# Kernel optimization log

Measured on AMD Instinct MI355X. Metric: run time of the kernel, lower is better.

Reference implementation:

```python
import jax, jax.numpy as jnp
import numpy as np

B, R, C, W, HEADS = 4, 32, 96, 4, 4
SHIFT = W // 2
N = W ** 3                      # tokens per window = 64
NW = (R // W) ** 3              # windows per sample = 512
MLP = 4 * C
EPS = 1e-5


def _build_attn_mask():
    img = np.zeros((R, R, R), dtype=np.float32)
    slices = (slice(0, -W), slice(-W, -SHIFT), slice(-SHIFT, None))
    cnt = 0
    for xs in slices:
        for ys in slices:
            for zs in slices:
                img[xs, ys, zs] = cnt
                cnt += 1
    m = img.reshape(R // W, W, R // W, W, R // W, W)
    m = m.transpose(0, 2, 4, 1, 3, 5).reshape(NW, N)          # (nW, N)
    diff = m[:, None, :] - m[:, :, None]                       # (nW, N, N)
    return np.where(diff != 0, -100.0, 0.0).astype(np.float32)


def setup_inputs() -> dict:
    key = jax.random.key(0)
    ks = jax.random.split(key, 8)
    s = 0.02
    return {
        "inputs": jax.random.normal(ks[0], (B, R ** 3, C), jnp.float32),
        "norm1_g": jnp.ones((C,), jnp.float32),
        "norm1_b": jnp.zeros((C,), jnp.float32),
        "qkv_w": jax.random.normal(ks[1], (C, 3 * C), jnp.float32) * s,
        "qkv_b": jnp.zeros((3 * C,), jnp.float32),
        "proj_w": jax.random.normal(ks[2], (C, C), jnp.float32) * s,
        "proj_b": jnp.zeros((C,), jnp.float32),
        "norm2_g": jnp.ones((C,), jnp.float32),
        "norm2_b": jnp.zeros((C,), jnp.float32),
        "mlp_w1": jax.random.normal(ks[3], (C, MLP), jnp.float32) * s,
        "mlp_b1": jnp.zeros((MLP,), jnp.float32),
        "mlp_w2": jax.random.normal(ks[4], (MLP, C), jnp.float32) * s,
        "mlp_b2": jnp.zeros((C,), jnp.float32),
        "attn_mask": jnp.asarray(_build_attn_mask()),
    }


def _layernorm(x, g, b):
    mu = jnp.mean(x, axis=-1, keepdims=True)
    var = jnp.mean(jnp.square(x - mu), axis=-1, keepdims=True)
    return (x - mu) * jax.lax.rsqrt(var + EPS) * g + b


def _box_partition(x):
    # (B, R, R, R, C) -> (B*nW, N, C)
    x = x.reshape(B, R // W, W, R // W, W, R // W, W, C)
    x = x.transpose(0, 1, 3, 5, 2, 4, 6, 7)
    return x.reshape(-1, N, C)


def _box_reverse(boxes):
    # (B*nW, N, C) -> (B, R, R, R, C)
    x = boxes.reshape(B, R // W, R // W, R // W, W, W, W, C)
    x = x.transpose(0, 1, 4, 2, 5, 3, 6, 7)
    return x.reshape(B, R, R, R, C)


def _forward(inputs, norm1_g, norm1_b, qkv_w, qkv_b, proj_w, proj_b,
             norm2_g, norm2_b, mlp_w1, mlp_b1, mlp_w2, mlp_b2, attn_mask):
    shortcut = inputs
    x = _layernorm(inputs, norm1_g, norm1_b)
    x = x.reshape(B, R, R, R, C)
    x = jnp.roll(x, shift=(-SHIFT, -SHIFT, -SHIFT), axis=(1, 2, 3))
    boxes = _box_partition(x)                                   # (B*nW, N, C)

    dh = C // HEADS
    qkv = boxes @ qkv_w + qkv_b                                 # (B*nW, N, 3C)
    qkv = qkv.reshape(-1, N, 3, HEADS, dh)
    q, k, v = qkv[:, :, 0], qkv[:, :, 1], qkv[:, :, 2]          # (B*nW, N, H, dh)
    scale = dh ** -0.5
    attn = jnp.einsum('wnhd,wmhd->whnm', q, k) * scale          # (B*nW, H, N, N)
    attn = attn.reshape(B, NW, HEADS, N, N) + attn_mask[None, :, None]
    attn = jax.nn.softmax(attn.reshape(-1, HEADS, N, N), axis=-1)
    out = jnp.einsum('whnm,wmhd->wnhd', attn, v).reshape(-1, N, C)
    out = out @ proj_w + proj_b                                 # (B*nW, N, C)

    x = _box_reverse(out)
    x = jnp.roll(x, shift=(SHIFT, SHIFT, SHIFT), axis=(1, 2, 3))
    x = x.reshape(B, R ** 3, C)
    x = x * 0.5 + shortcut                                      # drop_path=0 -> identity

    h = _layernorm(x, norm2_g, norm2_b)
    h = jax.nn.gelu(h @ mlp_w1 + mlp_b1) @ mlp_w2 + mlp_b2
    return h * 0.5 + x


def reference(inputs, norm1_g, norm1_b, qkv_w, qkv_b, proj_w, proj_b,
              norm2_g, norm2_b, mlp_w1, mlp_b1, mlp_w2, mlp_b2, attn_mask):
    return _forward(inputs, norm1_g, norm1_b, qkv_w, qkv_b, proj_w, proj_b,
                    norm2_g, norm2_b, mlp_w1, mlp_b1, mlp_w2, mlp_b2, attn_mask)
```

## Files before the change

### kernel.cpp

```cpp
#include <hip/hip_runtime.h>
#include <hip/hip_bf16.h>

#define CC 96
#define LDXP 104
#define KOFF 6656
#define XOFF 6656
#define VST 72

typedef __bf16 bf16;
typedef __attribute__((ext_vector_type(8))) __bf16 bf16x8;
typedef __attribute__((ext_vector_type(4))) float f32x4;

#define MFMA16(a, b, c) __builtin_amdgcn_mfma_f32_16x16x32_bf16(a, b, c, 0, 0, 0)

__device__ __attribute__((aligned(16))) bf16 g_w1t[384 * 96];
__device__ __attribute__((aligned(16))) bf16 g_w2t[96 * 384];
__device__ __attribute__((aligned(16))) bf16 g_qkvwt[288 * 96];
__device__ __attribute__((aligned(16))) bf16 g_projwt[96 * 96];

template<bool BF>
__device__ __forceinline__ float ldg(const void* p, size_t i) {
    if constexpr (BF) return (float)((const bf16*)p)[i];
    else              return ((const float*)p)[i];
}

template<bool BF>
__device__ __forceinline__ void ld24(const void* p, size_t base, float* v) {
    if constexpr (BF) {
        const bf16* q = (const bf16*)p + base;
        #pragma unroll
        for (int i = 0; i < 3; i++) {
            bf16x8 f = *(const bf16x8*)(q + i * 8);
            #pragma unroll
            for (int j = 0; j < 8; j++) v[i * 8 + j] = (float)f[j];
        }
    } else {
        #pragma unroll
        for (int i = 0; i < 24; i++) v[i] = ((const float*)p)[base + i];
    }
}

__device__ __forceinline__ void st24_lds(bf16* dst, const float* v) {
    #pragma unroll
    for (int i = 0; i < 3; i++) {
        bf16x8 f;
        #pragma unroll
        for (int j = 0; j < 8; j++) f[j] = (bf16)v[i * 8 + j];
        *(bf16x8*)(dst + i * 8) = f;
    }
}

template<bool BF>
__device__ __forceinline__ void st24_glob(const bf16* stage, void* out, size_t g) {
    if constexpr (BF) {
        #pragma unroll
        for (int i = 0; i < 3; i++)
            *(bf16x8*)((bf16*)out + g + i * 8) = *(const bf16x8*)(stage + i * 8);
    } else {
        #pragma unroll
        for (int i = 0; i < 6; i++) {
            f32x4 v;
            #pragma unroll
            for (int j = 0; j < 4; j++) v[j] = (float)stage[i * 4 + j];
            *(f32x4*)((float*)out + g + i * 4) = v;
        }
    }
}

__device__ __forceinline__ bf16x8 ldsA(const bf16* base, int row0, int ld, int k0) {
    const int l = threadIdx.x & 63;
    return *(const bf16x8*)(base + (row0 + (l & 15)) * ld + k0 + (l >> 4) * 8);
}
__device__ __forceinline__ bf16x8 gB(const bf16* base, int n0, int K, int k0) {
    const int l = threadIdx.x & 63;
    return *(const bf16x8*)(base + (n0 + (l & 15)) * K + k0 + (l >> 4) * 8);
}

__device__ __forceinline__ float gelu_f(float x) {
    const float s = x * x;
    const float r = x * __builtin_fmaf(0.044715f, s, 1.0f);
    return x * __builtin_amdgcn_rcpf(1.0f + __expf(-1.5957691216057308f * r));
}

template<bool BF>
__device__ void tbody(int idx, const void* qkv_w, const void* proj_w,
                      const void* w1, const void* w2) {
    if (idx < 384 * 96) {
        int n = idx / 96, k = idx % 96;
        g_w1t[idx] = (bf16)ldg<BF>(w1, (size_t)k * 384 + n);
    } else if (idx < 2 * 384 * 96) {
        int j = idx - 384 * 96; int n = j / 384, k = j % 384;
        g_w2t[j] = (bf16)ldg<BF>(w2, (size_t)k * 96 + n);
    } else if (idx < 2 * 384 * 96 + 288 * 96) {
        int j = idx - 2 * 384 * 96; int n = j / 96, k = j % 96;
        g_qkvwt[j] = (bf16)ldg<BF>(qkv_w, (size_t)k * 288 + n);
    } else {
        int j = idx - 2 * 384 * 96 - 288 * 96;
        if (j < 96 * 96) {
            int n = j / 96, k = j % 96;
            g_projwt[j] = (bf16)ldg<BF>(proj_w, (size_t)k * 96 + n);
        }
    }
}
__global__ __launch_bounds__(256) void transpose_kernel(
    const void* g1, const void* qkv_w, const void* proj_w, const void* w1, const void* w2) {
    const int idx = blockIdx.x * 256 + threadIdx.x;
    if (((const unsigned*)g1)[0] == 0x3F803F80u) tbody<true >(idx, qkv_w, proj_w, w1, w2);
    else                                         tbody<false>(idx, qkv_w, proj_w, w1, w2);
}

template<bool BF>
__device__ void fused_body(const void* x_in, const void* g1v, const void* b1v,
                           const void* qkv_b, const void* proj_b,
                           const void* g2v, const void* b2v, const void* mb1,
                           const void* mb2, void* out,
                           bf16* bufA, bf16* bufX, int* src_s)
{
    const int t = threadIdx.x;
    const int w = t >> 6;
    const int l = t & 63;
    const int box = blockIdx.x;
    const int b = box >> 9, bx = (box >> 6) & 7, by = (box >> 3) & 7, bz = box & 7;
    const bool b7x = (bx == 7), b7y = (by == 7), b7z = (bz == 7);
    const bool boundary = b7x || b7y || b7z;
    auto gc = [&](int n) -> int {
        return ((b7x && (n & 32)) ? 4 : 0) | ((b7y && (n & 8)) ? 2 : 0)
             | ((b7z && (n & 2)) ? 1 : 0);
    };
    const int qkvS = w * 4 + (w < 2 ? w : 2), qkvC = 5 - (w >> 1);
    const int sixS = w + (w < 2 ? w : 2),     sixC = 2 - (w >> 1);

    bf16x8 resid[3];

    if (t < 64) *(f32x4*)(bufX + t * LDXP + 96) = (f32x4){0.f, 0.f, 0.f, 0.f};

    {
        const int row = t >> 2, quad = t & 3;
        const int wx = row >> 4, wy = (row >> 2) & 3, wz = row & 3;
        const int sx = (bx * 4 + wx + 2) & 31;
        const int sy = (by * 4 + wy + 2) & 31;
        const int sz = (bz * 4 + wz + 2) & 31;
        const int src = ((b * 32 + sx) * 32 + sy) * 32 + sz;
        if (quad == 0) src_s[row] = src;
        float v[24];
        ld24<BF>(x_in, (size_t)src * CC + quad * 24, v);
        #pragma unroll
        for (int i = 0; i < 3; i++) {
            bf16x8 f;
            #pragma unroll
            for (int j = 0; j < 8; j++) f[j] = (bf16)v[i * 8 + j];
            resid[i] = f;
        }
        float s = 0.f, ss = 0.f;
        #pragma unroll
        for (int i = 0; i < 24; i++) { s += v[i]; ss += v[i] * v[i]; }
        s += __shfl_xor(s, 1);  ss += __shfl_xor(ss, 1);
        s += __shfl_xor(s, 2);  ss += __shfl_xor(ss, 2);
        const float mu = s * (1.f / 96.f);
        const float rstd = rsqrtf(ss * (1.f / 96.f) - mu * mu + 1e-5f);
        float o[24];
        #pragma unroll
        for (int i = 0; i < 24; i++) {
            const int c = quad * 24 + i;
            o[i] = (v[i] - mu) * rstd * ldg<BF>(g1v, c) + ldg<BF>(b1v, c);
        }
        st24_lds(bufA + row * LDXP + quad * 24, o);
    }
    __syncthreads();

    {
        bf16x8 aF[12];
        #pragma unroll
        for (int qt = 0; qt < 4; qt++)
            #pragma unroll
            for (int k = 0; k < 3; k++)
                aF[qt * 3 + k] = ldsA(bufA, qt * 16, LDXP, k * 32);
        __syncthreads();

        for (int i = 0; i < qkvC; i++) {
            const int nt = qkvS + i;
            const bf16x8 bB0 = gB(g_qkvwt, nt * 16, 96, 0);
            const bf16x8 bB1 = gB(g_qkvwt, nt * 16, 96, 32);
            const bf16x8 bB2 = gB(g_qkvwt, nt * 16, 96, 64);
            const int col = nt * 16 + (l & 15);
            const float bias = ldg<BF>(qkv_b, col);
            #pragma unroll
            for (int qt = 0; qt < 4; qt++) {
                f32x4 acc = {0.f, 0.f, 0.f, 0.f};
                acc = MFMA16(aF[qt * 3 + 0], bB0, acc);
                acc = MFMA16(aF[qt * 3 + 1], bB1, acc);
                acc = MFMA16(aF[qt * 3 + 2], bB2, acc);
                const int rq = qt * 16 + ((l >> 4) << 2);
                if (nt < 6) {
                    #pragma unroll
                    for (int r = 0; r < 4; r++)
                        bufX[(rq + r) * LDXP + col] = (bf16)(acc[r] + bias);
                } else if (nt < 12) {
                    const int c = col - 96;
                    #pragma unroll
                    for (int r = 0; r < 4; r++)
                        bufX[KOFF + (rq + r) * LDXP + c] = (bf16)(acc[r] + bias);
                } else {
                    const int c = col - 192;
                    #pragma unroll
                    for (int r = 0; r < 4; r++)
                        bufA[c * VST + rq + r] = (bf16)(acc[r] + bias);
                }
            }
        }
    }
    __syncthreads();

    {
        const int h = w;
        bf16x8 aQ[4], bK[4], bV[2][2];
        #pragma unroll
        for (int qt = 0; qt < 4; qt++)
            aQ[qt] = *(const bf16x8*)(bufX + (qt * 16 + (l & 15)) * LDXP + h * 24 + ((l >> 4) << 3));
        #pragma unroll
        for (int mt = 0; mt < 4; mt++) {
            if (l < 48) {
                bK[mt] = *(const bf16x8*)(bufX + KOFF + (mt * 16 + (l & 15)) * LDXP
                                          + h * 24 + ((l >> 4) << 3));
            } else {
                bf16x8 z;
                #pragma unroll
                for (int j = 0; j < 8; j++) z[j] = (bf16)0.f;
                bK[mt] = z;
            }
        }
        #pragma unroll
        for (int ks = 0; ks < 2; ks++)
            #pragma unroll
            for (int nt = 0; nt < 2; nt++)
                bV[ks][nt] = *(const bf16x8*)(bufA + (h * 24 + nt * 8 + (l & 15)) * VST
                                              + ks * 32 + ((l >> 4) << 3));
        __syncthreads();

        f32x4 S[4][4];
        #pragma unroll
        for (int qt = 0; qt < 4; qt++)
            #pragma unroll
            for (int mt = 0; mt < 4; mt++)
                S[qt][mt] = MFMA16(aQ[qt], bK[mt], ((f32x4){0.f, 0.f, 0.f, 0.f}));

        {
            const int row = t >> 2, quad = t & 3;
            #pragma unroll
            for (int i = 0; i < 3; i++)
                *(bf16x8*)(bufX + XOFF + row * LDXP + quad * 24 + i * 8) = resid[i];
        }

        const float scale = 0.20412414523193154f;
        bf16* pB = bufX + h * 1024;
        int gcol[4];
        if (boundary) {
            #pragma unroll
            for (int mt = 0; mt < 4; mt++) gcol[mt] = gc(mt * 16 + (l & 15));
        }
        #pragma unroll
        for (int qt = 0; qt < 4; qt++) {
            float e[4][4], rs[4] = {0.f, 0.f, 0.f, 0.f};
            if (boundary) {
                int grow[4];
                #pragma unroll
                for (int r = 0; r < 4; r++)
                    grow[r] = gc(qt * 16 + ((l >> 4) << 2) + r);
                #pragma unroll
                for (int mt = 0; mt < 4; mt++)
                    #pragma unroll
                    for (int r = 0; r < 4; r++) {
                        float ev = __expf(S[qt][mt][r] * scale);
                        ev = (grow[r] == gcol[mt]) ? ev : 0.f;
                        e[mt][r] = ev; rs[r] += ev;
                    }
            } else {
                #pragma unroll
                for (int mt = 0; mt < 4; mt++)
                    #pragma unroll
                    for (int r = 0; r < 4; r++) {
                        const float ev = __expf(S[qt][mt][r] * scale);
                        e[mt][r] = ev; rs[r] += ev;
                    }
            }
            #pragma unroll
            for (int r = 0; r < 4; r++) {
                rs[r] += __shfl_xor(rs[r], 1);
                rs[r] += __shfl_xor(rs[r], 2);
                rs[r] += __shfl_xor(rs[r], 4);
                rs[r] += __shfl_xor(rs[r], 8);
            }
            float ri[4];
            #pragma unroll
            for (int r = 0; r < 4; r++) ri[r] = __builtin_amdgcn_rcpf(rs[r]);
            #pragma unroll
            for (int mt = 0; mt < 4; mt++) {
                const int colm = mt * 16 + (l & 15);
                const int chl = colm >> 3;
                #pragma unroll
                for (int r = 0; r < 4; r++) {
                    const int lr = ((l >> 4) << 2) + r;
                    const int ch = chl ^ (lr & 7);
                    pB[lr * 64 + ch * 8 + (colm & 7)] = (bf16)(e[mt][r] * ri[r]);
                }
            }
            f32x4 Oq0 = {0.f, 0.f, 0.f, 0.f}, Oq1 = {0.f, 0.f, 0.f, 0.f};
            #pragma unroll
            for (int ks = 0; ks < 2; ks++) {
                const int lr2 = l & 15;
                const int ch = (ks * 4 + (l >> 4)) ^ (lr2 & 7);
                const bf16x8 aP = *(const bf16x8*)(pB + lr2 * 64 + ch * 8);
                Oq0 = MFMA16(aP, bV[ks][0], Oq0);
                Oq1 = MFMA16(aP, bV[ks][1], Oq1);
            }
            #pragma unroll
            for (int nt = 0; nt < 2; nt++) {
                const int cl = nt * 8 + (l & 15);
                if (nt == 0 || (l & 15) >= 8) {
                    const f32x4 Ov = nt ? Oq1 : Oq0;
                    #pragma unroll
                    for (int r = 0; r < 4; r++) {
                        const int row = qt * 16 + ((l >> 4) << 2) + r;
                        bufA[row * LDXP + h * 24 + cl] = (bf16)Ov[r];
                    }
                }
            }
        }
    }
    __syncthreads();

    {
        bf16x8 pF[12];
        #pragma unroll
        for (int qt = 0; qt < 4; qt++)
            #pragma unroll
            for (int k = 0; k < 3; k++)
                pF[qt * 3 + k] = ldsA(bufA, qt * 16, LDXP, k * 32);

        for (int i = 0; i < sixC; i++) {
            const int nt = sixS + i;
            const bf16x8 bB0 = gB(g_projwt, nt * 16, 96, 0);
            const bf16x8 bB1 = gB(g_projwt, nt * 16, 96, 32);
            const bf16x8 bB2 = gB(g_projwt, nt * 16, 96, 64);
            const int col = nt * 16 + (l & 15);
            const float bias = ldg<BF>(proj_b, col);
            #pragma unroll
            for (int qt = 0; qt < 4; qt++) {
                f32x4 acc = {0.f, 0.f, 0.f, 0.f};
                acc = MFMA16(pF[qt * 3 + 0], bB0, acc);
                acc = MFMA16(pF[qt * 3 + 1], bB1, acc);
                acc = MFMA16(pF[qt * 3 + 2], bB2, acc);
                const int rq = qt * 16 + ((l >> 4) << 2);
                #pragma unroll
                for (int r = 0; r < 4; r++) {
                    const int idx = XOFF + (rq + r) * LDXP + col;
                    const float x2v = 0.5f * (acc[r] + bias) + (float)bufX[idx];
                    bufX[idx] = (bf16)x2v;
                }
            }
        }
    }
    __syncthreads();

    {
        const int row = t >> 2, quad = t & 3;
        float v[24];
        #pragma unroll
        for (int i = 0; i < 3; i++) {
            bf16x8 f = *(const bf16x8*)(bufX + XOFF + row * LDXP + quad * 24 + i * 8);
            #pragma unroll
            for (int j = 0; j < 8; j++) v[i * 8 + j] = (float)f[j];
        }
        float s = 0.f, ss = 0.f;
        #pragma unroll
        for (int i = 0; i < 24; i++) { s += v[i]; ss += v[i] * v[i]; }
        s += __shfl_xor(s, 1);  ss += __shfl_xor(ss, 1);
        s += __shfl_xor(s, 2);  ss += __shfl_xor(ss, 2);
        const float mu = s * (1.f / 96.f);
        const float rstd = rsqrtf(ss * (1.f / 96.f) - mu * mu + 1e-5f);
        float o[24];
        #pragma unroll
        for (int i = 0; i < 24; i++) {
            const int c = quad * 24 + i;
            o[i] = (v[i] - mu) * rstd * ldg<BF>(g2v, c) + ldg<BF>(b2v, c);
        }
        st24_lds(bufX + row * LDXP + quad * 24, o);
    }
    __syncthreads();

    {
        bf16x8 mF[12];
        #pragma unroll
        for (int qt = 0; qt < 4; qt++)
            #pragma unroll
            for (int k = 0; k < 3; k++)
                mF[qt * 3 + k] = ldsA(bufX, qt * 16, LDXP, k * 32);

        f32x4 C[2][4];
        #pragma unroll
        for (int i = 0; i < 2; i++)
            #pragma unroll
            for (int qt = 0; qt < 4; qt++) C[i][qt] = (f32x4){0.f, 0.f, 0.f, 0.f};

        for (int c = 0; c < 4; c++) {
            if (c) __syncthreads();
            for (int i = 0; i < sixC; i++) {
                const int lt = sixS + i;
                const int n0 = c * 96 + lt * 16;
                const bf16x8 bB0 = gB(g_w1t, n0, 96, 0);
                const bf16x8 bB1 = gB(g_w1t, n0, 96, 32);
                const bf16x8 bB2 = gB(g_w1t, n0, 96, 64);
                const int colc = lt * 16 + (l & 15);
                const float bias = ldg<BF>(mb1, c * 96 + colc);
                #pragma unroll
                for (int qt = 0; qt < 4; qt++) {
                    f32x4 acc = {0.f, 0.f, 0.f, 0.f};
                    acc = MFMA16(mF[qt * 3 + 0], bB0, acc);
                    acc = MFMA16(mF[qt * 3 + 1], bB1, acc);
                    acc = MFMA16(mF[qt * 3 + 2], bB2, acc);
                    const int rq = qt * 16 + ((l >> 4) << 2);
                    #pragma unroll
                    for (int r = 0; r < 4; r++)
                        bufA[(rq + r) * LDXP + colc] = (bf16)gelu_f(acc[r] + bias);
                }
            }
            __syncthreads();
            bf16x8 hF[12];
            #pragma unroll
            for (int qt = 0; qt < 4; qt++) {
                hF[qt * 3 + 0] = ldsA(bufA, qt * 16, LDXP, 0);
                hF[qt * 3 + 1] = ldsA(bufA, qt * 16, LDXP, 32);
                hF[qt * 3 + 2] = ldsA(bufA, qt * 16, LDXP, 64);
            }
            for (int i = 0; i < sixC; i++) {
                const int ot = sixS + i;
                const bf16x8 bB0 = gB(g_w2t, ot * 16, 384, c * 96);
                const bf16x8 bB1 = gB(g_w2t, ot * 16, 384, c * 96 + 32);
                const bf16x8 bB2 = gB(g_w2t, ot * 16, 384, c * 96 + 64);
                #pragma unroll
                for (int qt = 0; qt < 4; qt++) {
                    C[i][qt] = MFMA16(hF[qt * 3 + 0], bB0, C[i][qt]);
                    C[i][qt] = MFMA16(hF[qt * 3 + 1], bB1, C[i][qt]);
                    C[i][qt] = MFMA16(hF[qt * 3 + 2], bB2, C[i][qt]);
                }
            }
        }
        __syncthreads();

        for (int i = 0; i < sixC; i++) {
            const int ot = sixS + i;
            const int col = ot * 16 + (l & 15);
            const float bias = ldg<BF>(mb2, col);
            #pragma unroll
            for (int qt = 0; qt < 4; qt++) {
                const int rq = qt * 16 + ((l >> 4) << 2);
                #pragma unroll
                for (int r = 0; r < 4; r++) {
                    const float res = (float)bufX[XOFF + (rq + r) * LDXP + col];
                    bufA[(rq + r) * LDXP + col] = (bf16)(0.5f * (C[i][qt][r] + bias) + res);
                }
            }
        }
        __syncthreads();
        {
            const int row = t >> 2, quad = t & 3;
            st24_glob<BF>(bufA + row * LDXP + quad * 24, out,
                          (size_t)src_s[row] * CC + quad * 24);
        }
    }
}

__global__ __launch_bounds__(256, 3) void fused_kernel(
    const void* x_in, const void* g1, const void* b1, const void* qkv_b,
    const void* proj_b, const void* g2, const void* b2,
    const void* mb1, const void* mb2, void* out) {
    __shared__ bf16 bufA[6912];
    __shared__ bf16 bufX[13312];
    __shared__ int src_s[64];
    if (((const unsigned*)g1)[0] == 0x3F803F80u)
        fused_body<true >(x_in, g1, b1, qkv_b, proj_b, g2, b2, mb1, mb2, out,
                          bufA, bufX, src_s);
    else
        fused_body<false>(x_in, g1, b1, qkv_b, proj_b, g2, b2, mb1, mb2, out,
                          bufA, bufX, src_s);
}

extern "C" void kernel_launch(void* const* d_in, const int* in_sizes, int n_in,
                              void* d_out, int out_size, void* d_ws, size_t ws_size,
                              hipStream_t stream) {
    const void* x_in   = d_in[0];
    const void* g1     = d_in[1];
    const void* b1     = d_in[2];
    const void* qkv_w  = d_in[3];
    const void* qkv_b  = d_in[4];
    const void* proj_w = d_in[5];
    const void* proj_b = d_in[6];
    const void* g2     = d_in[7];
    const void* b2     = d_in[8];
    const void* w1     = d_in[9];
    const void* bias1  = d_in[10];
    const void* w2     = d_in[11];
    const void* bias2  = d_in[12];

    transpose_kernel<<<432, 256, 0, stream>>>(g1, qkv_w, proj_w, w1, w2);
    fused_kernel<<<2048, 256, 0, stream>>>(x_in, g1, b1, qkv_b, proj_b,
                                           g2, b2, bias1, bias2, d_out);
}
```

Baseline: 212.0 us.

## Prefetch weight fragments across barriers and double-buffer loads in GEMM phases

Weight fragments and biases for the QKV, projection and MLP GEMMs are now loaded from global memory before the preceding barrier, or double-buffered one tile ahead. The per-wave tile loops are specialised on compile-time counts so they fully unroll. LayerNorm gamma and beta are loaded as vectors up front instead of one element at a time, and the fp32 input load is vectorised to float4. The aim is to hide global-load latency behind barriers and MFMA work, at the cost of more live registers and a possible drop in occupancy.

```diff
diff --git a/kernel.cpp b/kernel.cpp
--- a/kernel.cpp
+++ b/kernel.cpp
@@ -13,6 +13,8 @@
 
 #define MFMA16(a, b, c) __builtin_amdgcn_mfma_f32_16x16x32_bf16(a, b, c, 0, 0, 0)
 
+template<int N> struct icN { static constexpr int value = N; };
+
 __device__ __attribute__((aligned(16))) bf16 g_w1t[384 * 96];
 __device__ __attribute__((aligned(16))) bf16 g_w2t[96 * 384];
 __device__ __attribute__((aligned(16))) bf16 g_qkvwt[288 * 96];
@@ -35,8 +37,13 @@
             for (int j = 0; j < 8; j++) v[i * 8 + j] = (float)f[j];
         }
     } else {
-        #pragma unroll
-        for (int i = 0; i < 24; i++) v[i] = ((const float*)p)[base + i];
+        const float* q = (const float*)p + base;
+        #pragma unroll
+        for (int i = 0; i < 6; i++) {
+            f32x4 f = *(const f32x4*)(q + i * 4);
+            #pragma unroll
+            for (int j = 0; j < 4; j++) v[i * 4 + j] = f[j];
+        }
     }
 }
 
@@ -142,8 +149,10 @@
         const int sz = (bz * 4 + wz + 2) & 31;
         const int src = ((b * 32 + sx) * 32 + sy) * 32 + sz;
         if (quad == 0) src_s[row] = src;
-        float v[24];
+        float v[24], gv[24], bvv[24];
         ld24<BF>(x_in, (size_t)src * CC + quad * 24, v);
+        ld24<BF>(g1v, quad * 24, gv);
+        ld24<BF>(b1v, quad * 24, bvv);
         #pragma unroll
         for (int i = 0; i < 3; i++) {
             bf16x8 f;
@@ -160,12 +169,14 @@
         const float rstd = rsqrtf(ss * (1.f / 96.f) - mu * mu + 1e-5f);
         float o[24];
         #pragma unroll
-        for (int i = 0; i < 24; i++) {
-            const int c = quad * 24 + i;
-            o[i] = (v[i] - mu) * rstd * ldg<BF>(g1v, c) + ldg<BF>(b1v, c);
-        }
+        for (int i = 0; i < 24; i++)
+            o[i] = (v[i] - mu) * rstd * gv[i] + bvv[i];
         st24_lds(bufA + row * LDXP + quad * 24, o);
     }
+    bf16x8 q0f[3]; float q0b;
+    #pragma unroll
+    for (int k = 0; k < 3; k++) q0f[k] = gB(g_qkvwt, qkvS * 16, 96, k * 32);
+    q0b = ldg<BF>(qkv_b, qkvS * 16 + (l & 15));
     __syncthreads();
 
     {
@@ -177,37 +188,51 @@
                 aF[qt * 3 + k] = ldsA(bufA, qt * 16, LDXP, k * 32);
         __syncthreads();
 
-        for (int i = 0; i < qkvC; i++) {
-            const int nt = qkvS + i;
-            const bf16x8 bB0 = gB(g_qkvwt, nt * 16, 96, 0);
-            const bf16x8 bB1 = gB(g_qkvwt, nt * 16, 96, 32);
-            const bf16x8 bB2 = gB(g_qkvwt, nt * 16, 96, 64);
-            const int col = nt * 16 + (l & 15);
-            const float bias = ldg<BF>(qkv_b, col);
-            #pragma unroll
-            for (int qt = 0; qt < 4; qt++) {
-                f32x4 acc = {0.f, 0.f, 0.f, 0.f};
-                acc = MFMA16(aF[qt * 3 + 0], bB0, acc);
-                acc = MFMA16(aF[qt * 3 + 1], bB1, acc);
-                acc = MFMA16(aF[qt * 3 + 2], bB2, acc);
-                const int rq = qt * 16 + ((l >> 4) << 2);
-                if (nt < 6) {
-                    #pragma unroll
-                    for (int r = 0; r < 4; r++)
-                        bufX[(rq + r) * LDXP + col] = (bf16)(acc[r] + bias);
-                } else if (nt < 12) {
-                    const int c = col - 96;
-                    #pragma unroll
-                    for (int r = 0; r < 4; r++)
-                        bufX[KOFF + (rq + r) * LDXP + c] = (bf16)(acc[r] + bias);
-                } else {
-                    const int c = col - 192;
-                    #pragma unroll
-                    for (int r = 0; r < 4; r++)
-                        bufA[c * VST + rq + r] = (bf16)(acc[r] + bias);
-                }
-            }
-        }
+        auto qkv_phase = [&](auto cc) {
+            constexpr int CNT = decltype(cc)::value;
+            bf16x8 fb[2][3]; float bb[2];
+            #pragma unroll
+            for (int k = 0; k < 3; k++) fb[0][k] = q0f[k];
+            bb[0] = q0b;
+            #pragma unroll
+            for (int i = 0; i < CNT; i++) {
+                constexpr int dummy = 0; (void)dummy;
+                const int cur = i & 1, nxt = cur ^ 1;
+                if (i + 1 < CNT) {
+                    #pragma unroll
+                    for (int k = 0; k < 3; k++)
+                        fb[nxt][k] = gB(g_qkvwt, (qkvS + i + 1) * 16, 96, k * 32);
+                    bb[nxt] = ldg<BF>(qkv_b, (qkvS + i + 1) * 16 + (l & 15));
+                }
+                const int nt = qkvS + i;
+                const int col = nt * 16 + (l & 15);
+                #pragma unroll
+                for (int qt = 0; qt < 4; qt++) {
+                    f32x4 acc = {0.f, 0.f, 0.f, 0.f};
+                    acc = MFMA16(aF[qt * 3 + 0], fb[cur][0], acc);
+                    acc = MFMA16(aF[qt * 3 + 1], fb[cur][1], acc);
+                    acc = MFMA16(aF[qt * 3 + 2], fb[cur][2], acc);
+                    const int rq = qt * 16 + ((l >> 4) << 2);
+                    if (nt < 6) {
+                        #pragma unroll
+                        for (int r = 0; r < 4; r++)
+                            bufX[(rq + r) * LDXP + col] = (bf16)(acc[r] + bb[cur]);
+                    } else if (nt < 12) {
+                        const int c = col - 96;
+                        #pragma unroll
+                        for (int r = 0; r < 4; r++)
+                            bufX[KOFF + (rq + r) * LDXP + c] = (bf16)(acc[r] + bb[cur]);
+                    } else {
+                        const int c = col - 192;
+                        #pragma unroll
+                        for (int r = 0; r < 4; r++)
+                            bufA[c * VST + rq + r] = (bf16)(acc[r] + bb[cur]);
+                    }
+                }
+            }
+        };
+        if (w < 2) qkv_phase(icN<5>{});
+        else       qkv_phase(icN<4>{});
     }
     __syncthreads();
 
@@ -327,6 +352,21 @@
             }
         }
     }
+    bf16x8 pjB[2][3]; float pjb[2];
+    {
+        auto pload = [&](auto cc) {
+            constexpr int CNT = decltype(cc)::value;
+            #pragma unroll
+            for (int i = 0; i < CNT; i++) {
+                #pragma unroll
+                for (int k = 0; k < 3; k++)
+                    pjB[i][k] = gB(g_projwt, (sixS + i) * 16, 96, k * 32);
+                pjb[i] = ldg<BF>(proj_b, (sixS + i) * 16 + (l & 15));
+            }
+        };
+        if (w < 2) pload(icN<2>{});
+        else       pload(icN<1>{});
+    }
     __syncthreads();
 
     {
@@ -337,40 +377,44 @@
             for (int k = 0; k < 3; k++)
                 pF[qt * 3 + k] = ldsA(bufA, qt * 16, LDXP, k * 32);
 
-        for (int i = 0; i < sixC; i++) {
-            const int nt = sixS + i;
-            const bf16x8 bB0 = gB(g_projwt, nt * 16, 96, 0);
-            const bf16x8 bB1 = gB(g_projwt, nt * 16, 96, 32);
-            const bf16x8 bB2 = gB(g_projwt, nt * 16, 96, 64);
-            const int col = nt * 16 + (l & 15);
-            const float bias = ldg<BF>(proj_b, col);
-            #pragma unroll
-            for (int qt = 0; qt < 4; qt++) {
-                f32x4 acc = {0.f, 0.f, 0.f, 0.f};
-                acc = MFMA16(pF[qt * 3 + 0], bB0, acc);
-                acc = MFMA16(pF[qt * 3 + 1], bB1, acc);
-                acc = MFMA16(pF[qt * 3 + 2], bB2, acc);
-                const int rq = qt * 16 + ((l >> 4) << 2);
-                #pragma unroll
-                for (int r = 0; r < 4; r++) {
-                    const int idx = XOFF + (rq + r) * LDXP + col;
-                    const float x2v = 0.5f * (acc[r] + bias) + (float)bufX[idx];
-                    bufX[idx] = (bf16)x2v;
-                }
-            }
-        }
+        auto proj_phase = [&](auto cc) {
+            constexpr int CNT = decltype(cc)::value;
+            #pragma unroll
+            for (int i = 0; i < CNT; i++) {
+                const int nt = sixS + i;
+                const int col = nt * 16 + (l & 15);
+                #pragma unroll
+                for (int qt = 0; qt < 4; qt++) {
+                    f32x4 acc = {0.f, 0.f, 0.f, 0.f};
+                    acc = MFMA16(pF[qt * 3 + 0], pjB[i][0], acc);
+                    acc = MFMA16(pF[qt * 3 + 1], pjB[i][1], acc);
+                    acc = MFMA16(pF[qt * 3 + 2], pjB[i][2], acc);
+                    const int rq = qt * 16 + ((l >> 4) << 2);
+                    #pragma unroll
+                    for (int r = 0; r < 4; r++) {
+                        const int idx = XOFF + (rq + r) * LDXP + col;
+                        const float x2v = 0.5f * (acc[r] + pjb[i]) + (float)bufX[idx];
+                        bufX[idx] = (bf16)x2v;
+                    }
+                }
+            }
+        };
+        if (w < 2) proj_phase(icN<2>{});
+        else       proj_phase(icN<1>{});
     }
     __syncthreads();
 
     {
         const int row = t >> 2, quad = t & 3;
-        float v[24];
+        float v[24], gv[24], bvv[24];
         #pragma unroll
         for (int i = 0; i < 3; i++) {
             bf16x8 f = *(const bf16x8*)(bufX + XOFF + row * LDXP + quad * 24 + i * 8);
             #pragma unroll
             for (int j = 0; j < 8; j++) v[i * 8 + j] = (float)f[j];
         }
+        ld24<BF>(g2v, quad * 24, gv);
+        ld24<BF>(b2v, quad * 24, bvv);
         float s = 0.f, ss = 0.f;
         #pragma unroll
         for (int i = 0; i < 24; i++) { s += v[i]; ss += v[i] * v[i]; }
@@ -380,10 +424,8 @@
         const float rstd = rsqrtf(ss * (1.f / 96.f) - mu * mu + 1e-5f);
         float o[24];
         #pragma unroll
-        for (int i = 0; i < 24; i++) {
-            const int c = quad * 24 + i;
-            o[i] = (v[i] - mu) * rstd * ldg<BF>(g2v, c) + ldg<BF>(b2v, c);
-        }
+        for (int i = 0; i < 24; i++)
+            o[i] = (v[i] - mu) * rstd * gv[i] + bvv[i];
         st24_lds(bufX + row * LDXP + quad * 24, o);
     }
     __syncthreads();
@@ -402,48 +444,70 @@
             #pragma unroll
             for (int qt = 0; qt < 4; qt++) C[i][qt] = (f32x4){0.f, 0.f, 0.f, 0.f};
 
+        #pragma unroll
         for (int c = 0; c < 4; c++) {
+            bf16x8 fb[2][3]; float bb[2];
+            #pragma unroll
+            for (int k = 0; k < 3; k++)
+                fb[0][k] = gB(g_w1t, c * 96 + sixS * 16, 96, k * 32);
+            bb[0] = ldg<BF>(mb1, c * 96 + sixS * 16 + (l & 15));
             if (c) __syncthreads();
-            for (int i = 0; i < sixC; i++) {
-                const int lt = sixS + i;
-                const int n0 = c * 96 + lt * 16;
-                const bf16x8 bB0 = gB(g_w1t, n0, 96, 0);
-                const bf16x8 bB1 = gB(g_w1t, n0, 96, 32);
-                const bf16x8 bB2 = gB(g_w1t, n0, 96, 64);
-                const int colc = lt * 16 + (l & 15);
-                const float bias = ldg<BF>(mb1, c * 96 + colc);
+            auto mlp1_seg = [&](auto cc) {
+                constexpr int CNT = decltype(cc)::value;
+                #pragma unroll
+                for (int i = 0; i < CNT; i++) {
+                    const int cur = i & 1, nxt = cur ^ 1;
+                    if (i + 1 < CNT) {
+                        #pragma unroll
+                        for (int k = 0; k < 3; k++)
+                            fb[nxt][k] = gB(g_w1t, c * 96 + (sixS + i + 1) * 16, 96, k * 32);
+                        bb[nxt] = ldg<BF>(mb1, c * 96 + (sixS + i + 1) * 16 + (l & 15));
+                    }
+                    const int colc = (sixS + i) * 16 + (l & 15);
+                    #pragma unroll
+                    for (int qt = 0; qt < 4; qt++) {
+                        f32x4 acc = {0.f, 0.f, 0.f, 0.f};
+                        acc = MFMA16(mF[qt * 3 + 0], fb[cur][0], acc);
+                        acc = MFMA16(mF[qt * 3 + 1], fb[cur][1], acc);
+                        acc = MFMA16(mF[qt * 3 + 2], fb[cur][2], acc);
+                        const int rq = qt * 16 + ((l >> 4) << 2);
+                        #pragma unroll
+                        for (int r = 0; r < 4; r++)
+                            bufA[(rq + r) * LDXP + colc] = (bf16)gelu_f(acc[r] + bb[cur]);
+                    }
+                }
+            };
+            if (w < 2) mlp1_seg(icN<2>{});
+            else       mlp1_seg(icN<1>{});
+            bf16x8 w2f[2][3];
+            auto w2load = [&](auto cc) {
+                constexpr int CNT = decltype(cc)::value;
+                #pragma unroll
+                for (int i = 0; i < CNT; i++)
+                    #pragma unroll
+                    for (int k = 0; k < 3; k++)
+                        w2f[i][k] = gB(g_w2t, (sixS + i) * 16, 384, c * 96 + k * 32);
+            };
+            if (w < 2) w2load(icN<2>{});
+            else       w2load(icN<1>{});
+            __syncthreads();
+            auto mlp2_seg = [&](auto cc) {
+                constexpr int CNT = decltype(cc)::value;
                 #pragma unroll
                 for (int qt = 0; qt < 4; qt++) {
-                    f32x4 acc = {0.f, 0.f, 0.f, 0.f};
-                    acc = MFMA16(mF[qt * 3 + 0], bB0, acc);
-                    acc = MFMA16(mF[qt * 3 + 1], bB1, acc);
-                    acc = MFMA16(mF[qt * 3 + 2], bB2, acc);
-                    const int rq = qt * 16 + ((l >> 4) << 2);
-                    #pragma unroll
-                    for (int r = 0; r < 4; r++)
-                        bufA[(rq + r) * LDXP + colc] = (bf16)gelu_f(acc[r] + bias);
-                }
-            }
-            __syncthreads();
-            bf16x8 hF[12];
-            #pragma unroll
-            for (int qt = 0; qt < 4; qt++) {
-                hF[qt * 3 + 0] = ldsA(bufA, qt * 16, LDXP, 0);
-                hF[qt * 3 + 1] = ldsA(bufA, qt * 16, LDXP, 32);
-                hF[qt * 3 + 2] = ldsA(bufA, qt * 16, LDXP, 64);
-            }
-            for (int i = 0; i < sixC; i++) {
-                const int ot = sixS + i;
-                const bf16x8 bB0 = gB(g_w2t, ot * 16, 384, c * 96);
-                const bf16x8 bB1 = gB(g_w2t, ot * 16, 384, c * 96 + 32);
-                const bf16x8 bB2 = gB(g_w2t, ot * 16, 384, c * 96 + 64);
-                #pragma unroll
-                for (int qt = 0; qt < 4; qt++) {
-                    C[i][qt] = MFMA16(hF[qt * 3 + 0], bB0, C[i][qt]);
-                    C[i][qt] = MFMA16(hF[qt * 3 + 1], bB1, C[i][qt]);
-                    C[i][qt] = MFMA16(hF[qt * 3 + 2], bB2, C[i][qt]);
-                }
-            }
+                    const bf16x8 h0 = ldsA(bufA, qt * 16, LDXP, 0);
+                    const bf16x8 h1 = ldsA(bufA, qt * 16, LDXP, 32);
+                    const bf16x8 h2 = ldsA(bufA, qt * 16, LDXP, 64);
+                    #pragma unroll
+                    for (int i = 0; i < CNT; i++) {
+                        C[i][qt] = MFMA16(h0, w2f[i][0], C[i][qt]);
+                        C[i][qt] = MFMA16(h1, w2f[i][1], C[i][qt]);
+                        C[i][qt] = MFMA16(h2, w2f[i][2], C[i][qt]);
+                    }
+                }
+            };
+            if (w < 2) mlp2_seg(icN<2>{});
+            else       mlp2_seg(icN<1>{});
         }
         __syncthreads();
 
```

After: 248.5 us. 1.17x slower.

## Prefetch weight fragments across GEMM tiles and vectorize LayerNorm param loads

Applied to the files above, without the earlier changes.

Loads the next tile's global weight fragments and bias one iteration early in the QKV, projection and MLP-up loops, and issues the first tile's loads before the preceding barrier. This hides global-load latency behind the MFMA work. The MLP-down weights are loaded before the barrier, and the hidden fragments are read per row tile instead of being held in a 12-register array, which drops that array. The fp32 input path and the LayerNorm gamma/beta now use vector f32x4 loads into registers instead of scalar per-element loads. The prefetched fragments raise register pressure, which could hurt occupancy at the 3-blocks launch bound.

```diff
diff --git a/kernel.cpp b/kernel.cpp
--- a/kernel.cpp
+++ b/kernel.cpp
@@ -35,8 +35,13 @@
             for (int j = 0; j < 8; j++) v[i * 8 + j] = (float)f[j];
         }
     } else {
-        #pragma unroll
-        for (int i = 0; i < 24; i++) v[i] = ((const float*)p)[base + i];
+        const float* q = (const float*)p + base;
+        #pragma unroll
+        for (int i = 0; i < 6; i++) {
+            f32x4 f = *(const f32x4*)(q + i * 4);
+            #pragma unroll
+            for (int j = 0; j < 4; j++) v[i * 4 + j] = f[j];
+        }
     }
 }
 
@@ -142,8 +147,10 @@
         const int sz = (bz * 4 + wz + 2) & 31;
         const int src = ((b * 32 + sx) * 32 + sy) * 32 + sz;
         if (quad == 0) src_s[row] = src;
-        float v[24];
+        float v[24], gv[24], bvv[24];
         ld24<BF>(x_in, (size_t)src * CC + quad * 24, v);
+        ld24<BF>(g1v, quad * 24, gv);
+        ld24<BF>(b1v, quad * 24, bvv);
         #pragma unroll
         for (int i = 0; i < 3; i++) {
             bf16x8 f;
@@ -160,12 +167,14 @@
         const float rstd = rsqrtf(ss * (1.f / 96.f) - mu * mu + 1e-5f);
         float o[24];
         #pragma unroll
-        for (int i = 0; i < 24; i++) {
-            const int c = quad * 24 + i;
-            o[i] = (v[i] - mu) * rstd * ldg<BF>(g1v, c) + ldg<BF>(b1v, c);
-        }
+        for (int i = 0; i < 24; i++)
+            o[i] = (v[i] - mu) * rstd * gv[i] + bvv[i];
         st24_lds(bufA + row * LDXP + quad * 24, o);
     }
+    bf16x8 cf0 = gB(g_qkvwt, qkvS * 16, 96, 0);
+    bf16x8 cf1 = gB(g_qkvwt, qkvS * 16, 96, 32);
+    bf16x8 cf2 = gB(g_qkvwt, qkvS * 16, 96, 64);
+    float   cb = ldg<BF>(qkv_b, qkvS * 16 + (l & 15));
     __syncthreads();
 
     {
@@ -178,35 +187,39 @@
         __syncthreads();
 
         for (int i = 0; i < qkvC; i++) {
+            bf16x8 nf0 = cf0, nf1 = cf1, nf2 = cf2; float nb = cb;
+            if (i + 1 < qkvC) {
+                nf0 = gB(g_qkvwt, (qkvS + i + 1) * 16, 96, 0);
+                nf1 = gB(g_qkvwt, (qkvS + i + 1) * 16, 96, 32);
+                nf2 = gB(g_qkvwt, (qkvS + i + 1) * 16, 96, 64);
+                nb  = ldg<BF>(qkv_b, (qkvS + i + 1) * 16 + (l & 15));
+            }
             const int nt = qkvS + i;
-            const bf16x8 bB0 = gB(g_qkvwt, nt * 16, 96, 0);
-            const bf16x8 bB1 = gB(g_qkvwt, nt * 16, 96, 32);
-            const bf16x8 bB2 = gB(g_qkvwt, nt * 16, 96, 64);
             const int col = nt * 16 + (l & 15);
-            const float bias = ldg<BF>(qkv_b, col);
             #pragma unroll
             for (int qt = 0; qt < 4; qt++) {
                 f32x4 acc = {0.f, 0.f, 0.f, 0.f};
-                acc = MFMA16(aF[qt * 3 + 0], bB0, acc);
-                acc = MFMA16(aF[qt * 3 + 1], bB1, acc);
-                acc = MFMA16(aF[qt * 3 + 2], bB2, acc);
+                acc = MFMA16(aF[qt * 3 + 0], cf0, acc);
+                acc = MFMA16(aF[qt * 3 + 1], cf1, acc);
+                acc = MFMA16(aF[qt * 3 + 2], cf2, acc);
                 const int rq = qt * 16 + ((l >> 4) << 2);
                 if (nt < 6) {
                     #pragma unroll
                     for (int r = 0; r < 4; r++)
-                        bufX[(rq + r) * LDXP + col] = (bf16)(acc[r] + bias);
+                        bufX[(rq + r) * LDXP + col] = (bf16)(acc[r] + cb);
                 } else if (nt < 12) {
                     const int c = col - 96;
                     #pragma unroll
                     for (int r = 0; r < 4; r++)
-                        bufX[KOFF + (rq + r) * LDXP + c] = (bf16)(acc[r] + bias);
+                        bufX[KOFF + (rq + r) * LDXP + c] = (bf16)(acc[r] + cb);
                 } else {
                     const int c = col - 192;
                     #pragma unroll
                     for (int r = 0; r < 4; r++)
-                        bufA[c * VST + rq + r] = (bf16)(acc[r] + bias);
-                }
-            }
+                        bufA[c * VST + rq + r] = (bf16)(acc[r] + cb);
+                }
+            }
+            cf0 = nf0; cf1 = nf1; cf2 = nf2; cb = nb;
         }
     }
     __syncthreads();
@@ -327,6 +340,10 @@
             }
         }
     }
+    bf16x8 pc0 = gB(g_projwt, sixS * 16, 96, 0);
+    bf16x8 pc1 = gB(g_projwt, sixS * 16, 96, 32);
+    bf16x8 pc2 = gB(g_projwt, sixS * 16, 96, 64);
+    float  pcb = ldg<BF>(proj_b, sixS * 16 + (l & 15));
     __syncthreads();
 
     {
@@ -338,39 +355,45 @@
                 pF[qt * 3 + k] = ldsA(bufA, qt * 16, LDXP, k * 32);
 
         for (int i = 0; i < sixC; i++) {
+            bf16x8 nf0 = pc0, nf1 = pc1, nf2 = pc2; float nb = pcb;
+            if (i + 1 < sixC) {
+                nf0 = gB(g_projwt, (sixS + i + 1) * 16, 96, 0);
+                nf1 = gB(g_projwt, (sixS + i + 1) * 16, 96, 32);
+                nf2 = gB(g_projwt, (sixS + i + 1) * 16, 96, 64);
+                nb  = ldg<BF>(proj_b, (sixS + i + 1) * 16 + (l & 15));
+            }
             const int nt = sixS + i;
-            const bf16x8 bB0 = gB(g_projwt, nt * 16, 96, 0);
-            const bf16x8 bB1 = gB(g_projwt, nt * 16, 96, 32);
-            const bf16x8 bB2 = gB(g_projwt, nt * 16, 96, 64);
             const int col = nt * 16 + (l & 15);
-            const float bias = ldg<BF>(proj_b, col);
             #pragma unroll
             for (int qt = 0; qt < 4; qt++) {
                 f32x4 acc = {0.f, 0.f, 0.f, 0.f};
-                acc = MFMA16(pF[qt * 3 + 0], bB0, acc);
-                acc = MFMA16(pF[qt * 3 + 1], bB1, acc);
-                acc = MFMA16(pF[qt * 3 + 2], bB2, acc);
+                acc = MFMA16(pF[qt * 3 + 0], pc0, acc);
+                acc = MFMA16(pF[qt * 3 + 1], pc1, acc);
+                acc = MFMA16(pF[qt * 3 + 2], pc2, acc);
                 const int rq = qt * 16 + ((l >> 4) << 2);
                 #pragma unroll
                 for (int r = 0; r < 4; r++) {
                     const int idx = XOFF + (rq + r) * LDXP + col;
-                    const float x2v = 0.5f * (acc[r] + bias) + (float)bufX[idx];
+                    const float x2v = 0.5f * (acc[r] + pcb) + (float)bufX[idx];
                     bufX[idx] = (bf16)x2v;
                 }
             }
+            pc0 = nf0; pc1 = nf1; pc2 = nf2; pcb = nb;
         }
     }
     __syncthreads();
 
     {
         const int row = t >> 2, quad = t & 3;
-        float v[24];
+        float v[24], gv[24], bvv[24];
         #pragma unroll
         for (int i = 0; i < 3; i++) {
             bf16x8 f = *(const bf16x8*)(bufX + XOFF + row * LDXP + quad * 24 + i * 8);
             #pragma unroll
             for (int j = 0; j < 8; j++) v[i * 8 + j] = (float)f[j];
         }
+        ld24<BF>(g2v, quad * 24, gv);
+        ld24<BF>(b2v, quad * 24, bvv);
         float s = 0.f, ss = 0.f;
         #pragma unroll
         for (int i = 0; i < 24; i++) { s += v[i]; ss += v[i] * v[i]; }
@@ -380,10 +403,8 @@
         const float rstd = rsqrtf(ss * (1.f / 96.f) - mu * mu + 1e-5f);
         float o[24];
         #pragma unroll
-        for (int i = 0; i < 24; i++) {
-            const int c = quad * 24 + i;
-            o[i] = (v[i] - mu) * rstd * ldg<BF>(g2v, c) + ldg<BF>(b2v, c);
-        }
+        for (int i = 0; i < 24; i++)
+            o[i] = (v[i] - mu) * rstd * gv[i] + bvv[i];
         st24_lds(bufX + row * LDXP + quad * 24, o);
     }
     __syncthreads();
@@ -396,60 +417,70 @@
             for (int k = 0; k < 3; k++)
                 mF[qt * 3 + k] = ldsA(bufX, qt * 16, LDXP, k * 32);
 
-        f32x4 C[2][4];
-        #pragma unroll
-        for (int i = 0; i < 2; i++)
-            #pragma unroll
-            for (int qt = 0; qt < 4; qt++) C[i][qt] = (f32x4){0.f, 0.f, 0.f, 0.f};
+        f32x4 C0[4], C1[4];
+        #pragma unroll
+        for (int qt = 0; qt < 4; qt++) {
+            C0[qt] = (f32x4){0.f, 0.f, 0.f, 0.f};
+            C1[qt] = (f32x4){0.f, 0.f, 0.f, 0.f};
+        }
 
         for (int c = 0; c < 4; c++) {
+            bf16x8 m0 = gB(g_w1t, c * 96 + sixS * 16, 96, 0);
+            bf16x8 m1 = gB(g_w1t, c * 96 + sixS * 16, 96, 32);
+            bf16x8 m2 = gB(g_w1t, c * 96 + sixS * 16, 96, 64);
+            float  mb = ldg<BF>(mb1, c * 96 + sixS * 16 + (l & 15));
             if (c) __syncthreads();
             for (int i = 0; i < sixC; i++) {
-                const int lt = sixS + i;
-                const int n0 = c * 96 + lt * 16;
-                const bf16x8 bB0 = gB(g_w1t, n0, 96, 0);
-                const bf16x8 bB1 = gB(g_w1t, n0, 96, 32);
-                const bf16x8 bB2 = gB(g_w1t, n0, 96, 64);
-                const int colc = lt * 16 + (l & 15);
-                const float bias = ldg<BF>(mb1, c * 96 + colc);
+                bf16x8 n0 = m0, n1 = m1, n2 = m2; float nb = mb;
+                if (i + 1 < sixC) {
+                    n0 = gB(g_w1t, c * 96 + (sixS + i + 1) * 16, 96, 0);
+                    n1 = gB(g_w1t, c * 96 + (sixS + i + 1) * 16, 96, 32);
+                    n2 = gB(g_w1t, c * 96 + (sixS + i + 1) * 16, 96, 64);
+                    nb = ldg<BF>(mb1, c * 96 + (sixS + i + 1) * 16 + (l & 15));
+                }
+                const int colc = (sixS + i) * 16 + (l & 15);
                 #pragma unroll
                 for (int qt = 0; qt < 4; qt++) {
                     f32x4 acc = {0.f, 0.f, 0.f, 0.f};
-                    acc = MFMA16(mF[qt * 3 + 0], bB0, acc);
-                    acc = MFMA16(mF[qt * 3 + 1], bB1, acc);
-                    acc = MFMA16(mF[qt * 3 + 2], bB2, acc);
+                    acc = MFMA16(mF[qt * 3 + 0], m0, acc);
+                    acc = MFMA16(mF[qt * 3 + 1], m1, acc);
+                    acc = MFMA16(mF[qt * 3 + 2], m2, acc);
                     const int rq = qt * 16 + ((l >> 4) << 2);
                     #pragma unroll
                     for (int r = 0; r < 4; r++)
-                        bufA[(rq + r) * LDXP + colc] = (bf16)gelu_f(acc[r] + bias);
-                }
+                        bufA[(rq + r) * LDXP + colc] = (bf16)gelu_f(acc[r] + mb);
+                }
+                m0 = n0; m1 = n1; m2 = n2; mb = nb;
+            }
+            bf16x8 w2a0 = gB(g_w2t, sixS * 16, 384, c * 96);
+            bf16x8 w2a1 = gB(g_w2t, sixS * 16, 384, c * 96 + 32);
+            bf16x8 w2a2 = gB(g_w2t, sixS * 16, 384, c * 96 + 64);
+            bf16x8 w2b0 = w2a0, w2b1 = w2a1, w2b2 = w2a2;
+            if (sixC == 2) {
+                w2b0 = gB(g_w2t, (sixS + 1) * 16, 384, c * 96);
+                w2b1 = gB(g_w2t, (sixS + 1) * 16, 384, c * 96 + 32);
+                w2b2 = gB(g_w2t, (sixS + 1) * 16, 384, c * 96 + 64);
             }
             __syncthreads();
-            bf16x8 hF[12];
             #pragma unroll
             for (int qt = 0; qt < 4; qt++) {
-                hF[qt * 3 + 0] = ldsA(bufA, qt * 16, LDXP, 0);
-                hF[qt * 3 + 1] = ldsA(bufA, qt * 16, LDXP, 32);
-                hF[qt * 3 + 2] = ldsA(bufA, qt * 16, LDXP, 64);
-            }
-            for (int i = 0; i < sixC; i++) {
-                const int ot = sixS + i;
-                const bf16x8 bB0 = gB(g_w2t, ot * 16, 384, c * 96);
-                const bf16x8 bB1 = gB(g_w2t, ot * 16, 384, c * 96 + 32);
-                const bf16x8 bB2 = gB(g_w2t, ot * 16, 384, c * 96 + 64);
-                #pragma unroll
-                for (int qt = 0; qt < 4; qt++) {
-                    C[i][qt] = MFMA16(hF[qt * 3 + 0], bB0, C[i][qt]);
-                    C[i][qt] = MFMA16(hF[qt * 3 + 1], bB1, C[i][qt]);
-                    C[i][qt] = MFMA16(hF[qt * 3 + 2], bB2, C[i][qt]);
+                const bf16x8 h0 = ldsA(bufA, qt * 16, LDXP, 0);
+                const bf16x8 h1 = ldsA(bufA, qt * 16, LDXP, 32);
+                const bf16x8 h2 = ldsA(bufA, qt * 16, LDXP, 64);
+                C0[qt] = MFMA16(h0, w2a0, C0[qt]);
+                C0[qt] = MFMA16(h1, w2a1, C0[qt]);
+                C0[qt] = MFMA16(h2, w2a2, C0[qt]);
+                if (sixC == 2) {
+                    C1[qt] = MFMA16(h0, w2b0, C1[qt]);
+                    C1[qt] = MFMA16(h1, w2b1, C1[qt]);
+                    C1[qt] = MFMA16(h2, w2b2, C1[qt]);
                 }
             }
         }
         __syncthreads();
 
-        for (int i = 0; i < sixC; i++) {
-            const int ot = sixS + i;
-            const int col = ot * 16 + (l & 15);
+        {
+            const int col = sixS * 16 + (l & 15);
             const float bias = ldg<BF>(mb2, col);
             #pragma unroll
             for (int qt = 0; qt < 4; qt++) {
@@ -457,7 +488,20 @@
                 #pragma unroll
                 for (int r = 0; r < 4; r++) {
                     const float res = (float)bufX[XOFF + (rq + r) * LDXP + col];
-                    bufA[(rq + r) * LDXP + col] = (bf16)(0.5f * (C[i][qt][r] + bias) + res);
+                    bufA[(rq + r) * LDXP + col] = (bf16)(0.5f * (C0[qt][r] + bias) + res);
+                }
+            }
+        }
+        if (sixC == 2) {
+            const int col = (sixS + 1) * 16 + (l & 15);
+            const float bias = ldg<BF>(mb2, col);
+            #pragma unroll
+            for (int qt = 0; qt < 4; qt++) {
+                const int rq = qt * 16 + ((l >> 4) << 2);
+                #pragma unroll
+                for (int r = 0; r < 4; r++) {
+                    const float res = (float)bufX[XOFF + (rq + r) * LDXP + col];
+                    bufA[(rq + r) * LDXP + col] = (bf16)(0.5f * (C1[qt][r] + bias) + res);
                 }
             }
         }
```

Result: faster. 195.7 us (-7.7%).
